# Performance work log

Measured on AMD Instinct MI355X. Metric: run time of the kernel, lower is better.

The kernel has to match this reference:

```python
import jax, jax.numpy as jnp
import numpy as np

H = 1024          # frame height (template.shape[0])
W = 1024          # frame width  (template.shape[1])
CD = 900          # center_dims
MS = 10           # ms_h = ms_w
EPS = 1e-8
CS = (H - CD) // 2        # c_shp_x = c_shp_y = 62
OFF = MS + CS             # template crop offset = 72
TW = H - 2 * OFF          # cropped template side = 880
S = 2 * MS + 1            # NCC map side = 21


def setup_inputs() -> dict:
    key = jax.random.key(0)
    k1, k2 = jax.random.split(key)
    # spatially-correlated synthetic frame so the NCC peak is real (log-peak interpolation valid)
    noise = jax.random.normal(k1, (1, H, W, 1), jnp.float32)
    smooth = jax.lax.reduce_window(noise, 0.0, jax.lax.add, (1, 15, 15, 1), (1, 1, 1, 1), 'SAME') / 225.0
    template = smooth[0, :, :, 0]
    X = jnp.roll(template, (3, -2), axis=(0, 1))[None, :, :, None] \
        + 0.05 * jax.random.normal(k2, (1, H, W, 1), jnp.float32)
    return {"X": X, "template": template}


def _forward(X, template):
    # --- template normalization (zero-mean, variance) ---
    tmpl = template[OFF:H - OFF, OFF:W - OFF]                  # (TW, TW)
    t_zm = tmpl - jnp.mean(tmpl)
    t_var = jnp.sum(t_zm * t_zm) + EPS                         # scalar

    # --- image local normalization over the template window ---
    Xc = X[:, CS:H - CS, CS:W - CS, :]                         # (1, CD, CD, 1)
    imgs_zm = Xc - jnp.mean(Xc, axis=(1, 2), keepdims=True)
    win = (1, TW, TW, 1)
    ls = jax.lax.reduce_window(Xc, 0.0, jax.lax.add, win, (1, 1, 1, 1), 'VALID')        # local sum  (1,S,S,1)
    lsq = jax.lax.reduce_window(Xc * Xc, 0.0, jax.lax.add, win, (1, 1, 1, 1), 'VALID')  # local sumsq
    var = lsq - ls * ls / (TW * TW) + EPS
    var = jnp.maximum(var, 0.0)

    # --- NCC numerator: correlate zero-mean image with zero-mean template ---
    num = jax.lax.conv_general_dilated(
        imgs_zm, t_zm[:, :, None, None], (1, 1), 'VALID',
        dimension_numbers=('NHWC', 'HWIO', 'NHWC'))           # (1, S, S, 1)
    ncc = num / jnp.sqrt(t_var * var)
    ncc = jnp.where(jnp.isnan(ncc), 0.0, ncc)

    # --- subpixel peak via log-Gaussian interpolation ---
    ncc2 = ncc[0, :, :, 0]                                     # (S, S)
    idx = jnp.argmax(ncc2.reshape(-1))
    sx = (idx // S).astype(jnp.int32)
    sy = (idx % S).astype(jnp.int32)
    lg = jnp.log(ncc2)

    def at(r, c):
        return lg[jnp.clip(r, 0, S - 1), jnp.clip(c, 0, S - 1)]

    l_xm1, l_xp1 = at(sx - 1, sy), at(sx + 1, sy)
    l_ym1, l_yp1 = at(sx, sy - 1), at(sx, sy + 1)
    l4 = 4.0 * at(sx, sy)
    xs = -(sx.astype(jnp.float32) - MS) - (l_xm1 - l_xp1) / (2 * l_xm1 - l4 + 2 * l_xp1)
    ys = -(sy.astype(jnp.float32) - MS) - (l_ym1 - l_yp1) / (2 * l_ym1 - l4 + 2 * l_yp1)

    # --- bilinear translate (tfa.image.translate semantics: out[r,c] = in[r-xs, c-ys], fill 0) ---
    img = X[0, :, :, 0]
    rr = jnp.arange(H, dtype=jnp.float32) - xs
    cc = jnp.arange(W, dtype=jnp.float32) - ys
    r0 = jnp.floor(rr)
    c0 = jnp.floor(cc)
    wr = (rr - r0)[:, None]
    wc = (cc - c0)[None, :]
    r0i = r0.astype(jnp.int32)
    c0i = c0.astype(jnp.int32)

    def samp(ri, ci):
        vr = ((ri >= 0) & (ri < H))[:, None]
        vc = ((ci >= 0) & (ci < W))[None, :]
        v = img[jnp.clip(ri, 0, H - 1)[:, None], jnp.clip(ci, 0, W - 1)[None, :]]
        return jnp.where(vr & vc, v, 0.0)

    out = ((1 - wr) * (1 - wc) * samp(r0i, c0i)
           + (1 - wr) * wc * samp(r0i, c0i + 1)
           + wr * (1 - wc) * samp(r0i + 1, c0i)
           + wr * wc * samp(r0i + 1, c0i + 1))                 # (H, W)

    flat = out.T.reshape(-1)[None, :]                          # matches reshape(transpose(squeeze(.)), [-1])[None,:]
    return flat, xs, ys


def reference(X, template):
    flat, xs, ys = _forward(X, template)
    return (flat, xs, ys)
```

## Files before the change

### kernel.cpp

```cpp
#include <hip/hip_runtime.h>
#include <math.h>

#define HH 1024
#define WW 1024
#define CD 900
#define MS 10
#define CS 62
#define OFFT 72
#define TW 880
#define SS 21
#define EPSV 1e-8
#define NBAND 55
#define RPB 16
#define NCH 55


__global__ __launch_bounds__(256) void row_stats_kernel(const float* __restrict__ X,
                                                        const float* __restrict__ T,
                                                        float* __restrict__ RS1T,
                                                        float* __restrict__ RS2T,
                                                        float* __restrict__ Trow1,
                                                        float* __restrict__ Trow2,
                                                        float* __restrict__ Sfull) {
    const int b = blockIdx.x, tid = threadIdx.x;
    __shared__ float red[4][3];
    const int lane = tid & 63, wid = tid >> 6;
    if (b < CD) {
        const float* row = X + (size_t)(CS + b) * WW + CS;
        float sf = 0.f, sw = 0.f, qw = 0.f;
        for (int v = tid; v < CD; v += 256) {
            float x = row[v];
            sf += x;
            if (v < TW) { sw += x; qw += x * x; }
        }
        for (int m = 1; m < 64; m <<= 1) {
            sf += __shfl_xor(sf, m); sw += __shfl_xor(sw, m); qw += __shfl_xor(qw, m);
        }
        if (lane == 0) { red[wid][0] = sf; red[wid][1] = sw; red[wid][2] = qw; }
        __syncthreads();
        if (tid < 32) {
            const float swb = red[0][1] + red[1][1] + red[2][1] + red[3][1];
            const float qwb = red[0][2] + red[1][2] + red[2][2] + red[3][2];
            float d1 = 0.f, d2 = 0.f;
            if (tid >= 1 && tid < SS) {
                float a = row[tid - 1], c2 = row[TW + tid - 1];
                d1 = c2 - a;
                d2 = c2 * c2 - a * a;
            }
            for (int off = 1; off < 32; off <<= 1) {
                float u1 = __shfl_up(d1, off), u2 = __shfl_up(d2, off);
                if (tid >= off) { d1 += u1; d2 += u2; }
            }
            if (tid < SS) {
                RS1T[tid * CD + b] = swb + d1;
                RS2T[tid * CD + b] = qwb + d2;
            }
            if (tid == 0) Sfull[b] = red[0][0] + red[1][0] + red[2][0] + red[3][0];
        }
    } else {
        const int u = b - CD;
        const float* row = T + (size_t)(OFFT + u) * WW + OFFT;
        float s = 0.f, q = 0.f;
        for (int v = tid; v < TW; v += 256) { float t = row[v]; s += t; q += t * t; }
        for (int m = 1; m < 64; m <<= 1) { s += __shfl_xor(s, m); q += __shfl_xor(q, m); }
        if (lane == 0) { red[wid][0] = s; red[wid][1] = q; }
        __syncthreads();
        if (tid == 0) {
            Trow1[u] = red[0][0] + red[1][0] + red[2][0] + red[3][0];
            Trow2[u] = red[0][1] + red[1][1] + red[2][1] + red[3][1];
        }
    }
}

__global__ __launch_bounds__(256) void corr_kernel(const float* __restrict__ X,
                                                   const float* __restrict__ T,
                                                   float* __restrict__ part) {
    const int band = blockIdx.x, i = blockIdx.y;
    const int tid = threadIdx.x;
    const int u0 = band * RPB;

    float acc[SS];
#pragma unroll
    for (int j = 0; j < SS; ++j) acc[j] = 0.f;

#pragma unroll 1
    for (int item = tid; item < RPB * NCH; item += 256) {
        const int ul = item / NCH;
        const int c = item - ul * NCH;
        const int u = u0 + ul;
        const float4* xp = (const float4*)(X + (size_t)(CS + i + u) * WW + 60 + c * 16);
        const float4* tp = (const float4*)(T + (size_t)(OFFT + u) * WW + OFFT + c * 16);
        float xr[40], t[16];
#pragma unroll
        for (int k = 0; k < 10; ++k) {
            float4 q = xp[k];
            xr[4 * k] = q.x; xr[4 * k + 1] = q.y; xr[4 * k + 2] = q.z; xr[4 * k + 3] = q.w;
        }
#pragma unroll
        for (int k = 0; k < 4; ++k) {
            float4 q = tp[k];
            t[4 * k] = q.x; t[4 * k + 1] = q.y; t[4 * k + 2] = q.z; t[4 * k + 3] = q.w;
        }
#pragma unroll
        for (int j = 0; j < SS; ++j) {
            float a = acc[j];
#pragma unroll
            for (int k = 0; k < 16; ++k) a = fmaf(xr[2 + j + k], t[k], a);
            acc[j] = a;
        }
    }

#pragma unroll
    for (int j = 0; j < SS; ++j)
#pragma unroll
        for (int m = 1; m < 64; m <<= 1) acc[j] += __shfl_xor(acc[j], m);

    __shared__ float red[4][SS];
    const int lane = tid & 63, wid = tid >> 6;
    if (lane == 0) {
#pragma unroll
        for (int j = 0; j < SS; ++j) red[wid][j] = acc[j];
    }
    __syncthreads();
    if (tid < SS) {
        float s = red[0][tid] + red[1][tid] + red[2][tid] + red[3][tid];
        part[(i * NBAND + band) * SS + tid] = s;
    }
}

__global__ __launch_bounds__(256) void ncc_final_kernel(const float* __restrict__ part,
                                                        const float* __restrict__ RS1T,
                                                        const float* __restrict__ RS2T,
                                                        const float* __restrict__ Trow1,
                                                        const float* __restrict__ Trow2,
                                                        const float* __restrict__ Sfull,
                                                        float* __restrict__ ncc) {
    const int bid = blockIdx.x;
    const int i = bid / SS, j = bid - i * SS;
    const int tid = threadIdx.x;
    double dd = 0, d1 = 0, d2 = 0, ta = 0, tb = 0, xs = 0;
    for (int b = tid; b < NBAND; b += 256) dd += (double)part[(i * NBAND + b) * SS + j];
    const float* r1 = RS1T + j * CD + i;
    const float* r2 = RS2T + j * CD + i;
    for (int u = tid; u < TW; u += 256) {
        d1 += (double)r1[u]; d2 += (double)r2[u];
        ta += (double)Trow1[u]; tb += (double)Trow2[u];
    }
    for (int k = tid; k < CD; k += 256) xs += (double)Sfull[k];
    for (int m = 1; m < 64; m <<= 1) {
        dd += __shfl_xor(dd, m); d1 += __shfl_xor(d1, m); d2 += __shfl_xor(d2, m);
        ta += __shfl_xor(ta, m); tb += __shfl_xor(tb, m); xs += __shfl_xor(xs, m);
    }
    __shared__ double red[4][6];
    const int lane = tid & 63, wid = tid >> 6;
    if (lane == 0) {
        red[wid][0] = dd; red[wid][1] = d1; red[wid][2] = d2;
        red[wid][3] = ta; red[wid][4] = tb; red[wid][5] = xs;
    }
    __syncthreads();
    if (tid == 0) {
        double dot = red[0][0] + red[1][0] + red[2][0] + red[3][0];
        double S1  = red[0][1] + red[1][1] + red[2][1] + red[3][1];
        double S2  = red[0][2] + red[1][2] + red[2][2] + red[3][2];
        double sum_t  = red[0][3] + red[1][3] + red[2][3] + red[3][3];
        double sum_t2 = red[0][4] + red[1][4] + red[2][4] + red[3][4];
        double sumX   = red[0][5] + red[1][5] + red[2][5] + red[3][5];
        const double NT = 774400.0;
        double mt = sum_t / NT, mx = sumX / 810000.0;
        double tvar = sum_t2 - sum_t * sum_t / NT + EPSV;
        double var = S2 - S1 * S1 / NT + EPSV;
        if (var < 0.0) var = 0.0;
        double cross = dot - mt * S1 - mx * sum_t + NT * mx * mt;
        float val = (float)(cross / sqrt(tvar * var));
        if (isnan(val)) val = 0.f;
        ncc[i * SS + j] = val;
    }
}

__global__ __launch_bounds__(256) void shift_kernel(const float* __restrict__ img,
                                                    const float* __restrict__ ncc,
                                                    float* __restrict__ out) {
    __shared__ float sv[256];
    __shared__ int si[256];
    __shared__ float sxy[2];
    __shared__ float tile[64][65];
    const int tid = threadIdx.x;

    {
        float v = -1e30f; int vi = 0;
        for (int k = tid; k < SS * SS; k += 256) {
            float q = ncc[k];
            if (q > v) { v = q; vi = k; }
        }
        sv[tid] = v; si[tid] = vi;
        __syncthreads();
        for (int off = 128; off > 0; off >>= 1) {
            if (tid < off) {
                float v2 = sv[tid + off]; int i2 = si[tid + off];
                if (v2 > sv[tid] || (v2 == sv[tid] && i2 < si[tid])) { sv[tid] = v2; si[tid] = i2; }
            }
            __syncthreads();
        }
        if (tid == 0) {
            int idx = si[0];
            int sx = idx / SS;
            int sy = idx - sx * SS;
            auto at = [&](int r, int c) -> float {
                r = r < 0 ? 0 : (r > SS - 1 ? SS - 1 : r);
                c = c < 0 ? 0 : (c > SS - 1 ? SS - 1 : c);
                return logf(ncc[r * SS + c]);
            };
            float l4 = 4.0f * at(sx, sy);
            float lxm = at(sx - 1, sy), lxp = at(sx + 1, sy);
            float lym = at(sx, sy - 1), lyp = at(sx, sy + 1);
            float xsv = -((float)sx - (float)MS) - (lxm - lxp) / (2.0f * lxm - l4 + 2.0f * lxp);
            float ysv = -((float)sy - (float)MS) - (lym - lyp) / (2.0f * lym - l4 + 2.0f * lyp);
            sxy[0] = xsv; sxy[1] = ysv;
            if (blockIdx.x == 0 && blockIdx.y == 0) {
                out[(size_t)HH * WW] = xsv;
                out[(size_t)HH * WW + 1] = ysv;
            }
        }
        __syncthreads();
    }

    const float xs = sxy[0], ys = sxy[1];
    const int R0 = blockIdx.y * 64, C0 = blockIdx.x * 64;
    {
        const int cl = tid & 63, rg = tid >> 6;
        const int c = C0 + cl;
        const float cc = (float)c - ys;
        const float c0f = floorf(cc);
        const float wc = cc - c0f;
        const int c0 = (int)c0f;
        const bool vc0 = (c0 >= 0) & (c0 < WW);
        const bool vc1 = (c0 + 1 >= 0) & (c0 + 1 < WW);
        const int c0c = c0 < 0 ? 0 : (c0 > WW - 1 ? WW - 1 : c0);
        const int c1c = (c0 + 1) < 0 ? 0 : ((c0 + 1) > WW - 1 ? WW - 1 : c0 + 1);
        for (int k = 0; k < 16; ++k) {
            const int rl = rg * 16 + k;
            const int r = R0 + rl;
            const float rr = (float)r - xs;
            const float r0f = floorf(rr);
            const float wr = rr - r0f;
            const int r0 = (int)r0f;
            const bool vr0 = (r0 >= 0) & (r0 < HH);
            const bool vr1 = (r0 + 1 >= 0) & (r0 + 1 < HH);
            const int r0c = r0 < 0 ? 0 : (r0 > HH - 1 ? HH - 1 : r0);
            const int r1c = (r0 + 1) < 0 ? 0 : ((r0 + 1) > HH - 1 ? HH - 1 : r0 + 1);
            float s00 = img[(size_t)r0c * WW + c0c]; if (!(vr0 & vc0)) s00 = 0.f;
            float s01 = img[(size_t)r0c * WW + c1c]; if (!(vr0 & vc1)) s01 = 0.f;
            float s10 = img[(size_t)r1c * WW + c0c]; if (!(vr1 & vc0)) s10 = 0.f;
            float s11 = img[(size_t)r1c * WW + c1c]; if (!(vr1 & vc1)) s11 = 0.f;
            tile[rl][cl] = (1.f - wr) * (1.f - wc) * s00 + (1.f - wr) * wc * s01 +
                           wr * (1.f - wc) * s10 + wr * wc * s11;
        }
    }
    __syncthreads();
    {
        const int rl = tid & 63, cg = tid >> 6;
        for (int k = 0; k < 16; ++k) {
            const int cl = cg * 16 + k;
            out[(size_t)(C0 + cl) * HH + R0 + rl] = tile[rl][cl];
        }
    }
}

extern "C" void kernel_launch(void* const* d_in, const int* in_sizes, int n_in,
                              void* d_out, int out_size, void* d_ws, size_t ws_size,
                              hipStream_t stream) {
    const float* X = (const float*)d_in[0];
    const float* T = (const float*)d_in[1];
    float* out = (float*)d_out;

    char* w = (char*)d_ws;
    float* RS1T  = (float*)(w + 0);
    float* RS2T  = (float*)(w + 75600);
    float* Trow1 = (float*)(w + 151200);
    float* Trow2 = (float*)(w + 154720);
    float* Sfull = (float*)(w + 158240);
    float* part  = (float*)(w + 161840);
    float* ncc   = (float*)(w + 258880);

    row_stats_kernel<<<CD + TW, 256, 0, stream>>>(X, T, RS1T, RS2T, Trow1, Trow2, Sfull);
    corr_kernel<<<dim3(NBAND, SS), 256, 0, stream>>>(X, T, part);
    ncc_final_kernel<<<SS * SS, 256, 0, stream>>>(part, RS1T, RS2T, Trow1, Trow2, Sfull, ncc);
    shift_kernel<<<dim3(16, 16), 256, 0, stream>>>(X, ncc, out);
}
```

Baseline: 101.0 us.

## Fuse stats with correlation, single-block finalize with argmax, slim shift kernel

Merges the row-statistics and correlation kernels into one launch over a concatenated grid, so the two independent phases run concurrently and one launch disappears. The 441-block NCC reduction becomes a single 1024-thread block. It builds the sliding-window sums incrementally from prefix differences instead of re-summing 880 entries per output, then does the argmax and subpixel fit once. The shift kernel now just reads the two precomputed offsets instead of having all 256 blocks redo the argmax. The risk is that the single-block finalize serializes work on one CU.

```diff
diff --git a/kernel.cpp b/kernel.cpp
--- a/kernel.cpp
+++ b/kernel.cpp
@@ -13,218 +13,249 @@
 #define NBAND 55
 #define RPB 16
 #define NCH 55
-
-
-__global__ __launch_bounds__(256) void row_stats_kernel(const float* __restrict__ X,
+#define NPAIR 441
+#define NCORR (NBAND * SS)
+
+
+__global__ __launch_bounds__(256) void fused_corr_stats(const float* __restrict__ X,
                                                         const float* __restrict__ T,
                                                         float* __restrict__ RS1T,
                                                         float* __restrict__ RS2T,
                                                         float* __restrict__ Trow1,
                                                         float* __restrict__ Trow2,
-                                                        float* __restrict__ Sfull) {
-    const int b = blockIdx.x, tid = threadIdx.x;
-    __shared__ float red[4][3];
+                                                        float* __restrict__ Sfull,
+                                                        float* __restrict__ part) {
+    const int bx = blockIdx.x;
+    const int tid = threadIdx.x;
     const int lane = tid & 63, wid = tid >> 6;
-    if (b < CD) {
-        const float* row = X + (size_t)(CS + b) * WW + CS;
-        float sf = 0.f, sw = 0.f, qw = 0.f;
-        for (int v = tid; v < CD; v += 256) {
-            float x = row[v];
-            sf += x;
-            if (v < TW) { sw += x; qw += x * x; }
-        }
-        for (int m = 1; m < 64; m <<= 1) {
-            sf += __shfl_xor(sf, m); sw += __shfl_xor(sw, m); qw += __shfl_xor(qw, m);
-        }
-        if (lane == 0) { red[wid][0] = sf; red[wid][1] = sw; red[wid][2] = qw; }
+    __shared__ float red[4][SS];
+
+    if (bx < NCORR) {
+        const int i = bx / NBAND;
+        const int band = bx - i * NBAND;
+        const int u0 = band * RPB;
+
+        float acc[SS];
+#pragma unroll
+        for (int j = 0; j < SS; ++j) acc[j] = 0.f;
+
+#pragma unroll 1
+        for (int item = tid; item < RPB * NCH; item += 256) {
+            const int ul = item / NCH;
+            const int c = item - ul * NCH;
+            const int u = u0 + ul;
+            const float4* xp = (const float4*)(X + (size_t)(CS + i + u) * WW + 60 + c * 16);
+            const float4* tp = (const float4*)(T + (size_t)(OFFT + u) * WW + OFFT + c * 16);
+            float xr[40], t[16];
+#pragma unroll
+            for (int k = 0; k < 10; ++k) {
+                float4 q = xp[k];
+                xr[4 * k] = q.x; xr[4 * k + 1] = q.y; xr[4 * k + 2] = q.z; xr[4 * k + 3] = q.w;
+            }
+#pragma unroll
+            for (int k = 0; k < 4; ++k) {
+                float4 q = tp[k];
+                t[4 * k] = q.x; t[4 * k + 1] = q.y; t[4 * k + 2] = q.z; t[4 * k + 3] = q.w;
+            }
+#pragma unroll
+            for (int j = 0; j < SS; ++j) {
+                float a = acc[j];
+#pragma unroll
+                for (int k = 0; k < 16; ++k) a = fmaf(xr[2 + j + k], t[k], a);
+                acc[j] = a;
+            }
+        }
+
+#pragma unroll
+        for (int j = 0; j < SS; ++j)
+#pragma unroll
+            for (int m = 1; m < 64; m <<= 1) acc[j] += __shfl_xor(acc[j], m);
+
+        if (lane == 0) {
+#pragma unroll
+            for (int j = 0; j < SS; ++j) red[wid][j] = acc[j];
+        }
         __syncthreads();
-        if (tid < 32) {
-            const float swb = red[0][1] + red[1][1] + red[2][1] + red[3][1];
-            const float qwb = red[0][2] + red[1][2] + red[2][2] + red[3][2];
-            float d1 = 0.f, d2 = 0.f;
-            if (tid >= 1 && tid < SS) {
-                float a = row[tid - 1], c2 = row[TW + tid - 1];
-                d1 = c2 - a;
-                d2 = c2 * c2 - a * a;
-            }
-            for (int off = 1; off < 32; off <<= 1) {
-                float u1 = __shfl_up(d1, off), u2 = __shfl_up(d2, off);
-                if (tid >= off) { d1 += u1; d2 += u2; }
-            }
-            if (tid < SS) {
-                RS1T[tid * CD + b] = swb + d1;
-                RS2T[tid * CD + b] = qwb + d2;
-            }
-            if (tid == 0) Sfull[b] = red[0][0] + red[1][0] + red[2][0] + red[3][0];
+        if (tid < SS) {
+            float s = red[0][tid] + red[1][tid] + red[2][tid] + red[3][tid];
+            part[(i * NBAND + band) * SS + tid] = s;
         }
     } else {
-        const int u = b - CD;
-        const float* row = T + (size_t)(OFFT + u) * WW + OFFT;
-        float s = 0.f, q = 0.f;
-        for (int v = tid; v < TW; v += 256) { float t = row[v]; s += t; q += t * t; }
-        for (int m = 1; m < 64; m <<= 1) { s += __shfl_xor(s, m); q += __shfl_xor(q, m); }
-        if (lane == 0) { red[wid][0] = s; red[wid][1] = q; }
-        __syncthreads();
-        if (tid == 0) {
-            Trow1[u] = red[0][0] + red[1][0] + red[2][0] + red[3][0];
-            Trow2[u] = red[0][1] + red[1][1] + red[2][1] + red[3][1];
+        const int b = bx - NCORR;
+        if (b < CD) {
+            const float* row = X + (size_t)(CS + b) * WW + CS;
+            float sf = 0.f, sw = 0.f, qw = 0.f;
+            for (int v = tid; v < CD; v += 256) {
+                float x = row[v];
+                sf += x;
+                if (v < TW) { sw += x; qw += x * x; }
+            }
+            for (int m = 1; m < 64; m <<= 1) {
+                sf += __shfl_xor(sf, m); sw += __shfl_xor(sw, m); qw += __shfl_xor(qw, m);
+            }
+            if (lane == 0) { red[wid][0] = sf; red[wid][1] = sw; red[wid][2] = qw; }
+            __syncthreads();
+            if (tid < 32) {
+                const float swb = red[0][1] + red[1][1] + red[2][1] + red[3][1];
+                const float qwb = red[0][2] + red[1][2] + red[2][2] + red[3][2];
+                float d1 = 0.f, d2 = 0.f;
+                if (tid >= 1 && tid < SS) {
+                    float a = row[tid - 1], c2 = row[TW + tid - 1];
+                    d1 = c2 - a;
+                    d2 = c2 * c2 - a * a;
+                }
+                for (int off = 1; off < 32; off <<= 1) {
+                    float u1 = __shfl_up(d1, off), u2 = __shfl_up(d2, off);
+                    if (tid >= off) { d1 += u1; d2 += u2; }
+                }
+                if (tid < SS) {
+                    RS1T[tid * CD + b] = swb + d1;
+                    RS2T[tid * CD + b] = qwb + d2;
+                }
+                if (tid == 0) Sfull[b] = red[0][0] + red[1][0] + red[2][0] + red[3][0];
+            }
+        } else {
+            const int u = b - CD;
+            const float* row = T + (size_t)(OFFT + u) * WW + OFFT;
+            float s = 0.f, q = 0.f;
+            for (int v = tid; v < TW; v += 256) { float t = row[v]; s += t; q += t * t; }
+            for (int m = 1; m < 64; m <<= 1) { s += __shfl_xor(s, m); q += __shfl_xor(q, m); }
+            if (lane == 0) { red[wid][0] = s; red[wid][1] = q; }
+            __syncthreads();
+            if (tid == 0) {
+                Trow1[u] = red[0][0] + red[1][0] + red[2][0] + red[3][0];
+                Trow2[u] = red[0][1] + red[1][1] + red[2][1] + red[3][1];
+            }
         }
     }
 }
 
-__global__ __launch_bounds__(256) void corr_kernel(const float* __restrict__ X,
-                                                   const float* __restrict__ T,
-                                                   float* __restrict__ part) {
-    const int band = blockIdx.x, i = blockIdx.y;
-    const int tid = threadIdx.x;
-    const int u0 = band * RPB;
-
-    float acc[SS];
-#pragma unroll
-    for (int j = 0; j < SS; ++j) acc[j] = 0.f;
-
-#pragma unroll 1
-    for (int item = tid; item < RPB * NCH; item += 256) {
-        const int ul = item / NCH;
-        const int c = item - ul * NCH;
-        const int u = u0 + ul;
-        const float4* xp = (const float4*)(X + (size_t)(CS + i + u) * WW + 60 + c * 16);
-        const float4* tp = (const float4*)(T + (size_t)(OFFT + u) * WW + OFFT + c * 16);
-        float xr[40], t[16];
-#pragma unroll
-        for (int k = 0; k < 10; ++k) {
-            float4 q = xp[k];
-            xr[4 * k] = q.x; xr[4 * k + 1] = q.y; xr[4 * k + 2] = q.z; xr[4 * k + 3] = q.w;
-        }
-#pragma unroll
-        for (int k = 0; k < 4; ++k) {
-            float4 q = tp[k];
-            t[4 * k] = q.x; t[4 * k + 1] = q.y; t[4 * k + 2] = q.z; t[4 * k + 3] = q.w;
-        }
-#pragma unroll
-        for (int j = 0; j < SS; ++j) {
-            float a = acc[j];
-#pragma unroll
-            for (int k = 0; k < 16; ++k) a = fmaf(xr[2 + j + k], t[k], a);
-            acc[j] = a;
-        }
-    }
-
-#pragma unroll
-    for (int j = 0; j < SS; ++j)
-#pragma unroll
-        for (int m = 1; m < 64; m <<= 1) acc[j] += __shfl_xor(acc[j], m);
-
-    __shared__ float red[4][SS];
-    const int lane = tid & 63, wid = tid >> 6;
-    if (lane == 0) {
-#pragma unroll
-        for (int j = 0; j < SS; ++j) red[wid][j] = acc[j];
-    }
-    __syncthreads();
-    if (tid < SS) {
-        float s = red[0][tid] + red[1][tid] + red[2][tid] + red[3][tid];
-        part[(i * NBAND + band) * SS + tid] = s;
-    }
-}
-
-__global__ __launch_bounds__(256) void ncc_final_kernel(const float* __restrict__ part,
+__global__ __launch_bounds__(1024) void finalize_kernel(const float* __restrict__ part,
                                                         const float* __restrict__ RS1T,
                                                         const float* __restrict__ RS2T,
                                                         const float* __restrict__ Trow1,
                                                         const float* __restrict__ Trow2,
                                                         const float* __restrict__ Sfull,
-                                                        float* __restrict__ ncc) {
-    const int bid = blockIdx.x;
-    const int i = bid / SS, j = bid - i * SS;
-    const int tid = threadIdx.x;
-    double dd = 0, d1 = 0, d2 = 0, ta = 0, tb = 0, xs = 0;
-    for (int b = tid; b < NBAND; b += 256) dd += (double)part[(i * NBAND + b) * SS + j];
-    const float* r1 = RS1T + j * CD + i;
-    const float* r2 = RS2T + j * CD + i;
-    for (int u = tid; u < TW; u += 256) {
-        d1 += (double)r1[u]; d2 += (double)r2[u];
-        ta += (double)Trow1[u]; tb += (double)Trow2[u];
-    }
-    for (int k = tid; k < CD; k += 256) xs += (double)Sfull[k];
-    for (int m = 1; m < 64; m <<= 1) {
-        dd += __shfl_xor(dd, m); d1 += __shfl_xor(d1, m); d2 += __shfl_xor(d2, m);
-        ta += __shfl_xor(ta, m); tb += __shfl_xor(tb, m); xs += __shfl_xor(xs, m);
-    }
-    __shared__ double red[4][6];
-    const int lane = tid & 63, wid = tid >> 6;
-    if (lane == 0) {
-        red[wid][0] = dd; red[wid][1] = d1; red[wid][2] = d2;
-        red[wid][3] = ta; red[wid][4] = tb; red[wid][5] = xs;
+                                                        float* __restrict__ sxy,
+                                                        float* __restrict__ out) {
+    const int tid = threadIdx.x, lane = tid & 63, wid = tid >> 6;
+    __shared__ double sh_b1[SS], sh_b2[SS], sh_scal[3];
+    __shared__ double sh_dot[NPAIR];
+    __shared__ double sh_d1[420], sh_d2[420];
+    __shared__ double sh_S1[NPAIR], sh_S2[NPAIR];
+    __shared__ float nccs[NPAIR];
+    __shared__ float sv[1024];
+    __shared__ int si[1024];
+
+    {
+        const int j = wid;
+        const float* r1 = RS1T + j * CD;
+        const float* r2 = RS2T + j * CD;
+        double s1 = 0, s2 = 0;
+        for (int u = lane; u < TW; u += 64) { s1 += (double)r1[u]; s2 += (double)r2[u]; }
+        for (int m = 1; m < 64; m <<= 1) { s1 += __shfl_xor(s1, m); s2 += __shfl_xor(s2, m); }
+        if (lane == 0) { sh_b1[j] = s1; sh_b2[j] = s2; }
+    }
+    if (wid < 5) {
+        const int j = 16 + wid;
+        const float* r1 = RS1T + j * CD;
+        const float* r2 = RS2T + j * CD;
+        double s1 = 0, s2 = 0;
+        for (int u = lane; u < TW; u += 64) { s1 += (double)r1[u]; s2 += (double)r2[u]; }
+        for (int m = 1; m < 64; m <<= 1) { s1 += __shfl_xor(s1, m); s2 += __shfl_xor(s2, m); }
+        if (lane == 0) { sh_b1[j] = s1; sh_b2[j] = s2; }
+    } else if (wid == 5) {
+        double s = 0, q = 0;
+        for (int u = lane; u < TW; u += 64) { s += (double)Trow1[u]; q += (double)Trow2[u]; }
+        for (int m = 1; m < 64; m <<= 1) { s += __shfl_xor(s, m); q += __shfl_xor(q, m); }
+        if (lane == 0) { sh_scal[0] = s; sh_scal[1] = q; }
+    } else if (wid == 6) {
+        double s = 0;
+        for (int u = lane; u < CD; u += 64) s += (double)Sfull[u];
+        for (int m = 1; m < 64; m <<= 1) s += __shfl_xor(s, m);
+        if (lane == 0) sh_scal[2] = s;
+    }
+
+    if (tid < NPAIR) {
+        const int i = tid / SS, j = tid - i * SS;
+        double dv = 0;
+        for (int b = 0; b < NBAND; ++b) dv += (double)part[(i * NBAND + b) * SS + j];
+        sh_dot[tid] = dv;
+    } else if (tid < NPAIR + 420) {
+        const int q = tid - NPAIR;
+        const int ii = q / SS + 1;
+        const int j = q - (ii - 1) * SS;
+        sh_d1[q] = (double)RS1T[j * CD + ii + 879] - (double)RS1T[j * CD + ii - 1];
+        sh_d2[q] = (double)RS2T[j * CD + ii + 879] - (double)RS2T[j * CD + ii - 1];
     }
     __syncthreads();
-    if (tid == 0) {
-        double dot = red[0][0] + red[1][0] + red[2][0] + red[3][0];
-        double S1  = red[0][1] + red[1][1] + red[2][1] + red[3][1];
-        double S2  = red[0][2] + red[1][2] + red[2][2] + red[3][2];
-        double sum_t  = red[0][3] + red[1][3] + red[2][3] + red[3][3];
-        double sum_t2 = red[0][4] + red[1][4] + red[2][4] + red[3][4];
-        double sumX   = red[0][5] + red[1][5] + red[2][5] + red[3][5];
+
+    if (tid < SS) {
+        const int j = tid;
+        double w1 = sh_b1[j], w2 = sh_b2[j];
+        sh_S1[j] = w1; sh_S2[j] = w2;
+        for (int i2 = 1; i2 < SS; ++i2) {
+            w1 += sh_d1[(i2 - 1) * SS + j];
+            w2 += sh_d2[(i2 - 1) * SS + j];
+            sh_S1[i2 * SS + j] = w1;
+            sh_S2[i2 * SS + j] = w2;
+        }
+    }
+    __syncthreads();
+
+    float val = -1e30f;
+    if (tid < NPAIR) {
         const double NT = 774400.0;
-        double mt = sum_t / NT, mx = sumX / 810000.0;
-        double tvar = sum_t2 - sum_t * sum_t / NT + EPSV;
+        const double dot = sh_dot[tid], S1 = sh_S1[tid], S2 = sh_S2[tid];
+        const double sum_t = sh_scal[0], sum_t2 = sh_scal[1], sumX = sh_scal[2];
+        const double mt = sum_t / NT, mx = sumX / 810000.0;
+        const double tvar = sum_t2 - sum_t * sum_t / NT + EPSV;
         double var = S2 - S1 * S1 / NT + EPSV;
         if (var < 0.0) var = 0.0;
-        double cross = dot - mt * S1 - mx * sum_t + NT * mx * mt;
-        float val = (float)(cross / sqrt(tvar * var));
-        if (isnan(val)) val = 0.f;
-        ncc[i * SS + j] = val;
+        const double cross = dot - mt * S1 - mx * sum_t + NT * mx * mt;
+        float v = (float)(cross / sqrt(tvar * var));
+        if (isnan(v)) v = 0.f;
+        nccs[tid] = v;
+        val = v;
+    }
+    sv[tid] = val; si[tid] = tid;
+    __syncthreads();
+
+    for (int off = 512; off > 0; off >>= 1) {
+        if (tid < off) {
+            float v2 = sv[tid + off]; int i2 = si[tid + off];
+            if (v2 > sv[tid] || (v2 == sv[tid] && i2 < si[tid])) { sv[tid] = v2; si[tid] = i2; }
+        }
+        __syncthreads();
+    }
+
+    if (tid == 0) {
+        const int idx = si[0];
+        const int sx = idx / SS;
+        const int sy = idx - sx * SS;
+        auto at = [&](int r, int c) -> float {
+            r = r < 0 ? 0 : (r > SS - 1 ? SS - 1 : r);
+            c = c < 0 ? 0 : (c > SS - 1 ? SS - 1 : c);
+            return logf(nccs[r * SS + c]);
+        };
+        const float l4 = 4.0f * at(sx, sy);
+        const float lxm = at(sx - 1, sy), lxp = at(sx + 1, sy);
+        const float lym = at(sx, sy - 1), lyp = at(sx, sy + 1);
+        const float xsv = -((float)sx - (float)MS) - (lxm - lxp) / (2.0f * lxm - l4 + 2.0f * lxp);
+        const float ysv = -((float)sy - (float)MS) - (lym - lyp) / (2.0f * lym - l4 + 2.0f * lyp);
+        sxy[0] = xsv; sxy[1] = ysv;
+        out[(size_t)HH * WW] = xsv;
+        out[(size_t)HH * WW + 1] = ysv;
     }
 }
 
 __global__ __launch_bounds__(256) void shift_kernel(const float* __restrict__ img,
-                                                    const float* __restrict__ ncc,
+                                                    const float* __restrict__ sxy,
                                                     float* __restrict__ out) {
-    __shared__ float sv[256];
-    __shared__ int si[256];
-    __shared__ float sxy[2];
     __shared__ float tile[64][65];
     const int tid = threadIdx.x;
-
-    {
-        float v = -1e30f; int vi = 0;
-        for (int k = tid; k < SS * SS; k += 256) {
-            float q = ncc[k];
-            if (q > v) { v = q; vi = k; }
-        }
-        sv[tid] = v; si[tid] = vi;
-        __syncthreads();
-        for (int off = 128; off > 0; off >>= 1) {
-            if (tid < off) {
-                float v2 = sv[tid + off]; int i2 = si[tid + off];
-                if (v2 > sv[tid] || (v2 == sv[tid] && i2 < si[tid])) { sv[tid] = v2; si[tid] = i2; }
-            }
-            __syncthreads();
-        }
-        if (tid == 0) {
-            int idx = si[0];
-            int sx = idx / SS;
-            int sy = idx - sx * SS;
-            auto at = [&](int r, int c) -> float {
-                r = r < 0 ? 0 : (r > SS - 1 ? SS - 1 : r);
-                c = c < 0 ? 0 : (c > SS - 1 ? SS - 1 : c);
-                return logf(ncc[r * SS + c]);
-            };
-            float l4 = 4.0f * at(sx, sy);
-            float lxm = at(sx - 1, sy), lxp = at(sx + 1, sy);
-            float lym = at(sx, sy - 1), lyp = at(sx, sy + 1);
-            float xsv = -((float)sx - (float)MS) - (lxm - lxp) / (2.0f * lxm - l4 + 2.0f * lxp);
-            float ysv = -((float)sy - (float)MS) - (lym - lyp) / (2.0f * lym - l4 + 2.0f * lyp);
-            sxy[0] = xsv; sxy[1] = ysv;
-            if (blockIdx.x == 0 && blockIdx.y == 0) {
-                out[(size_t)HH * WW] = xsv;
-                out[(size_t)HH * WW + 1] = ysv;
-            }
-        }
-        __syncthreads();
-    }
-
     const float xs = sxy[0], ys = sxy[1];
+
     const int R0 = blockIdx.y * 64, C0 = blockIdx.x * 64;
     {
         const int cl = tid & 63, rg = tid >> 6;
@@ -280,10 +311,9 @@
     float* Trow2 = (float*)(w + 154720);
     float* Sfull = (float*)(w + 158240);
     float* part  = (float*)(w + 161840);
-    float* ncc   = (float*)(w + 258880);
-
-    row_stats_kernel<<<CD + TW, 256, 0, stream>>>(X, T, RS1T, RS2T, Trow1, Trow2, Sfull);
-    corr_kernel<<<dim3(NBAND, SS), 256, 0, stream>>>(X, T, part);
-    ncc_final_kernel<<<SS * SS, 256, 0, stream>>>(part, RS1T, RS2T, Trow1, Trow2, Sfull, ncc);
-    shift_kernel<<<dim3(16, 16), 256, 0, stream>>>(X, ncc, out);
+    float* sxy   = (float*)(w + 258880);
+
+    fused_corr_stats<<<NCORR + CD + TW, 256, 0, stream>>>(X, T, RS1T, RS2T, Trow1, Trow2, Sfull, part);
+    finalize_kernel<<<1, 1024, 0, stream>>>(part, RS1T, RS2T, Trow1, Trow2, Sfull, sxy, out);
+    shift_kernel<<<dim3(16, 16), 256, 0, stream>>>(X, sxy, out);
 }
```

Result: slower. 106.3 us (+5.3%).
